# Performance work log

Hardware: AMD Instinct MI355X
Metric: run time of the kernel (lower is better)

The kernel has to match this reference:

```python
import jax, jax.numpy as jnp
import numpy as np

B, S, D, H = 2, 2048, 1024, 16
Dh = D // H
ROPE_BASE = 10000.0


def _rope_cos_sin(seq_len, dh, dtype):
    inv_freq = 1.0 / (ROPE_BASE ** (jnp.arange(0, dh, 2, dtype=jnp.float32) / dh))
    t = jnp.arange(seq_len, dtype=jnp.float32)
    freqs = jnp.outer(t, inv_freq)              # (S, Dh/2)
    emb = jnp.concatenate([freqs, freqs], -1)   # (S, Dh)
    return jnp.cos(emb).astype(dtype), jnp.sin(emb).astype(dtype)


def _rotate_half(x):
    x1, x2 = jnp.split(x, 2, axis=-1)
    return jnp.concatenate([-x2, x1], axis=-1)


def setup_inputs() -> dict:
    key = jax.random.key(0)
    k1, k2, k3 = jax.random.split(key, 3)
    x = jax.random.normal(k1, (B, S, D), dtype=jnp.float32)
    w_qkv = jax.random.normal(k2, (D, 3 * D), dtype=jnp.float32) * (1.0 / np.sqrt(D))
    w_proj = jax.random.normal(k3, (D, D), dtype=jnp.float32) * (1.0 / np.sqrt(D))
    return {"x": x, "w_qkv": w_qkv, "w_proj": w_proj}


def reference(x, w_qkv, w_proj):
    b, s, d = x.shape
    qkv = x @ w_qkv                              # (B, S, 3D)
    q, k, v = jnp.split(qkv, 3, axis=-1)
    # (B, S, D) -> (B, H, S, Dh)
    shape_heads = lambda t: t.reshape(b, s, H, Dh).transpose(0, 2, 1, 3)
    q, k, v = shape_heads(q), shape_heads(k), shape_heads(v)
    cos, sin = _rope_cos_sin(s, Dh, x.dtype)     # (S, Dh) each
    cos = cos[None, None]                        # (1,1,S,Dh)
    sin = sin[None, None]
    q = q * cos + _rotate_half(q) * sin
    k = k * cos + _rotate_half(k) * sin
    attn = jnp.einsum('bhqd,bhkd->bhqk', q, k) / np.sqrt(Dh).astype(x.dtype)
    causal_mask = jnp.tril(jnp.ones((s, s), dtype=bool))
    attn = jnp.where(causal_mask, attn, -jnp.inf)
    attn = jax.nn.softmax(attn, axis=-1)
    out = jnp.einsum('bhqk,bhkd->bhqd', attn, v)
    out = out.transpose(0, 2, 1, 3).reshape(b, s, d)
    return out @ w_proj
```

## Files before the change

kernel.cpp:

```cpp
#include <hip/hip_runtime.h>


typedef unsigned short u16;
typedef unsigned int u32;
typedef __bf16 bf16x8 __attribute__((ext_vector_type(8)));
typedef unsigned short u16x8 __attribute__((ext_vector_type(8)));
typedef unsigned short u16x4 __attribute__((ext_vector_type(4)));
typedef float f32x4 __attribute__((ext_vector_type(4)));

#define B_ 2
#define S_ 2048
#define D_ 1024
#define H_ 16
#define DH_ 64
#define BS_ (B_ * S_)
#define N3_ (3 * D_)

__device__ __forceinline__ u16 f2bf(float f) {
  unsigned u = __float_as_uint(f);
  u += 0x7FFFu + ((u >> 16) & 1u);
  return (u16)(u >> 16);
}
__device__ __forceinline__ float bf2f(u16 s) {
  return __uint_as_float(((unsigned)s) << 16);
}

union BU { u16x8 u; bf16x8 b; };

__device__ __forceinline__ void gl16(const void* g, void* l) {
  __builtin_amdgcn_global_load_lds(
      (const __attribute__((address_space(1))) u32*)g,
      (__attribute__((address_space(3))) u32*)l, 16, 0, 0);
}

__global__ __launch_bounds__(256) void k_pre(const float* __restrict__ x,
                                             const float* __restrict__ wqkv,
                                             const float* __restrict__ wproj,
                                             u16* __restrict__ xb,
                                             u16* __restrict__ wqkvT,
                                             u16* __restrict__ wprojT,
                                             float* __restrict__ ct,
                                             float* __restrict__ st) {
  __shared__ float tl[32][33];
  const int bid = blockIdx.x;
  const int t = threadIdx.x;
  if (bid < 4096) {
    const int i = bid * 256 + t;
    const float4 f = ((const float4*)x)[i];
    u16x4 o;
    o[0] = f2bf(f.x); o[1] = f2bf(f.y); o[2] = f2bf(f.z); o[3] = f2bf(f.w);
    *(u16x4*)(xb + (size_t)i * 4) = o;
    return;
  }
  if (bid < 8192) {
    const float* w; u16* wT; int R, C, bx, by;
    if (bid < 7168) {
      w = wqkv; wT = wqkvT; R = D_; C = N3_;
      const int id2 = bid - 4096; bx = id2 % 96; by = id2 / 96;
    } else {
      w = wproj; wT = wprojT; R = D_; C = D_;
      const int id2 = bid - 7168; bx = id2 % 32; by = id2 / 32;
    }
    const int lrow = t >> 3, seg = t & 7;
    const int r0 = by * 32, c0 = bx * 32;
    const float4 f = *(const float4*)(w + (size_t)(r0 + lrow) * C + c0 + seg * 4);
    tl[lrow][seg * 4 + 0] = f.x; tl[lrow][seg * 4 + 1] = f.y;
    tl[lrow][seg * 4 + 2] = f.z; tl[lrow][seg * 4 + 3] = f.w;
    __syncthreads();
    u16x4 o;
#pragma unroll
    for (int j = 0; j < 4; ++j) o[j] = f2bf(tl[seg * 4 + j][lrow]);
    *(u16x4*)(wT + (size_t)(c0 + lrow) * R + r0 + seg * 4) = o;
    return;
  }
  {
    const int idx = (bid - 8192) * 256 + t;
    const int tpos = idx >> 5, i = idx & 31;
    const float invf = powf(10000.0f, -(float)i * (1.0f / 32.0f));
    const float a = (float)tpos * invf;
    ct[idx] = cosf(a);
    st[idx] = sinf(a);
  }
}

template <typename OutT>
__global__ __launch_bounds__(256) void k_gemm(const u16* __restrict__ A,
                                              const u16* __restrict__ BT,
                                              OutT* __restrict__ C,
                                              int M, int N, int K, int nbx) {
  __shared__ u16 smem[16384];
  u16* laA = smem;
  u16* laB = smem + 8192;
  const int t = threadIdx.x;
  const int per_x = gridDim.x >> 3;
  const int nid = (blockIdx.x & 7) * per_x + (blockIdx.x >> 3);
  const int n0 = (nid % nbx) * 128, m0 = (nid / nbx) * 128;
  const int w = t >> 6, lane = t & 63;
  const int lr = lane & 15, lg = lane >> 4;
  const int wm = (w >> 1) * 64, wn = (w & 1) * 64;
  const int NK = K >> 5;

  const int srow = lane >> 2;
  const int sc = ((lane & 3) ^ ((lane >> 3) & 3)) * 8;
  const u16* Ag = A + (size_t)(m0 + w * 32 + srow) * K + sc;
  const u16* Bg = BT + (size_t)(n0 + w * 32 + srow) * K + sc;
  const int ldsw = w * 1024;

  f32x4 acc[4][4] = {};

#pragma unroll
  for (int i = 0; i < 2; ++i) {
    gl16(Ag + (size_t)i * 16 * K, laA + ldsw + i * 512);
    gl16(Bg + (size_t)i * 16 * K, laB + ldsw + i * 512);
  }
  __syncthreads();

  int cur = 0;
  for (int kt = 0; kt < NK; ++kt) {
    if (kt + 1 < NK) {
      const int ko = (kt + 1) * 32;
#pragma unroll
      for (int i = 0; i < 2; ++i) {
        gl16(Ag + (size_t)i * 16 * K + ko, laA + (cur ^ 1) * 4096 + ldsw + i * 512);
        gl16(Bg + (size_t)i * 16 * K + ko, laB + (cur ^ 1) * 4096 + ldsw + i * 512);
      }
    }
    const char* pa = (const char*)(laA + cur * 4096);
    const char* pb = (const char*)(laB + cur * 4096);
    BU af[4], bfr[4];
    const int rsw = ((lr >> 1) & 3);
#pragma unroll
    for (int mi = 0; mi < 4; ++mi) {
      const int ra = wm + mi * 16 + lr;
      af[mi].u = *(const u16x8*)(pa + ra * 64 + ((lg ^ rsw) * 16));
      const int rb = wn + mi * 16 + lr;
      bfr[mi].u = *(const u16x8*)(pb + rb * 64 + ((lg ^ rsw) * 16));
    }
#pragma unroll
    for (int mi = 0; mi < 4; ++mi)
#pragma unroll
      for (int ni = 0; ni < 4; ++ni)
        acc[mi][ni] = __builtin_amdgcn_mfma_f32_16x16x32_bf16(af[mi].b, bfr[ni].b,
                                                              acc[mi][ni], 0, 0, 0);
    __syncthreads();
    cur ^= 1;
  }

  if constexpr (sizeof(OutT) == 2) {
    u16* ew = smem + w * 4096;
#pragma unroll
    for (int mi = 0; mi < 4; ++mi)
#pragma unroll
      for (int ni = 0; ni < 4; ++ni)
#pragma unroll
        for (int r = 0; r < 4; ++r)
          ew[(mi * 16 + lg * 4 + r) * 64 + ni * 16 + lr] = f2bf(acc[mi][ni][r]);
    const int er = lane >> 3, es = (lane & 7) * 8;
#pragma unroll
    for (int pass = 0; pass < 8; ++pass) {
      const int row = pass * 8 + er;
      const u16x8 v = *(const u16x8*)(ew + row * 64 + es);
      *(u16x8*)((u16*)C + (size_t)(m0 + wm + row) * N + n0 + wn + es) = v;
    }
  } else {
#pragma unroll
    for (int mi = 0; mi < 4; ++mi)
#pragma unroll
      for (int ni = 0; ni < 4; ++ni)
#pragma unroll
        for (int r = 0; r < 4; ++r) {
          const int row = m0 + wm + mi * 16 + lg * 4 + r;
          const int col = n0 + wn + ni * 16 + lr;
          ((float*)C)[(size_t)row * N + col] = acc[mi][ni][r];
        }
  }
}

__global__ __launch_bounds__(256) void k_prep(const u16* __restrict__ qkv,
                                              const float* __restrict__ ct,
                                              const float* __restrict__ st,
                                              u16* __restrict__ Q, u16* __restrict__ K,
                                              u16* __restrict__ Vt) {
  __shared__ u16 vl[64][72];
  const int bid = blockIdx.x;
  const int xcd = bid & 7, slot = bid >> 3;
  const int bh = xcd + 8 * (slot >> 5);
  const int stile = slot & 31;
  const int b = bh >> 4, h = bh & 15;
  const int t = threadIdx.x;
  const int row = t >> 2, qr = t & 3;
  const int s = stile * 64 + row;
  const u16* base = qkv + (size_t)(b * S_ + s) * N3_ + h * DH_;
  const int d0 = qr * 8;
  float c[8], sn[8];
#pragma unroll
  for (int j = 0; j < 8; ++j) {
    c[j] = ct[s * 32 + d0 + j];
    sn[j] = st[s * 32 + d0 + j];
  }
#pragma unroll
  for (int part = 0; part < 2; ++part) {
    const float qs = (part == 0) ? 0.125f : 1.0f;
    const u16* src = base + part * D_;
    u16x8 lo = *(const u16x8*)(src + d0);
    u16x8 hi = *(const u16x8*)(src + d0 + 32);
    u16x8 olo, ohi;
#pragma unroll
    for (int j = 0; j < 8; ++j) {
      float x1 = bf2f(lo[j]) * qs, x2 = bf2f(hi[j]) * qs;
      olo[j] = f2bf(x1 * c[j] - x2 * sn[j]);
      ohi[j] = f2bf(x2 * c[j] + x1 * sn[j]);
    }
    u16* dst = (part ? K : Q) + ((size_t)bh * S_ + s) * DH_;
    *(u16x8*)(dst + d0) = olo;
    *(u16x8*)(dst + d0 + 32) = ohi;
  }
  u16x8 v0 = *(const u16x8*)(base + 2 * D_ + qr * 16);
  u16x8 v1 = *(const u16x8*)(base + 2 * D_ + qr * 16 + 8);
#pragma unroll
  for (int j = 0; j < 8; ++j) {
    vl[qr * 16 + j][row] = v0[j];
    vl[qr * 16 + 8 + j][row] = v1[j];
  }
  __syncthreads();
  const int dh = row, sc = qr * 16;
  u16x8 o0, o1;
#pragma unroll
  for (int j = 0; j < 8; ++j) { o0[j] = vl[dh][sc + j]; o1[j] = vl[dh][sc + 8 + j]; }
  u16* vdst = Vt + ((size_t)bh * DH_ + dh) * S_ + stile * 64 + sc;
  *(u16x8*)vdst = o0;
  *(u16x8*)(vdst + 8) = o1;
}

__global__ __launch_bounds__(256, 2) void k_attn(const u16* __restrict__ Q,
                                                 const u16* __restrict__ K,
                                                 const u16* __restrict__ Vt,
                                                 u16* __restrict__ Ao) {
  __shared__ char kvb_[2][16384];
  __shared__ char plb[4][2048];
  const int bid = blockIdx.x;
  const int xcd = bid & 7, inner = bid >> 3;
  const int bh = xcd + 8 * (inner & 3);
  const int qt = 31 - (inner >> 2);
  const int t = threadIdx.x;
  const int w = t >> 6, lane = t & 63;
  const int lr = lane & 15, lg = lane >> 4;
  const int q0 = qt * 64 + w * 16;
  const int nt = qt + 1;

  const u16* Kbh = K + (size_t)bh * S_ * DH_;
  const u16* Vbh = Vt + (size_t)bh * DH_ * S_;

  const int sr = lane >> 3;
  const int sc = ((lane & 7) ^ sr) * 8;
  char* kd0 = kvb_[0] + w * 2048;
  char* kd1 = kvb_[1] + w * 2048;

  const u16* Qb = Q + ((size_t)bh * S_ + q0) * DH_;
  BU qf0, qf1;
  qf0.u = *(const u16x8*)(Qb + lr * DH_ + lg * 8);
  qf1.u = *(const u16x8*)(Qb + lr * DH_ + 32 + lg * 8);

  f32x4 o[4] = {};
  float m = -1e30f, l = 0.f;
  char* plw = plb[w];
  const int psw = (lr & 7) << 4;

#pragma unroll
  for (int j = 0; j < 2; ++j) {
    const int row = w * 16 + j * 8 + sr;
    gl16(Kbh + (size_t)row * DH_ + sc, kd0 + j * 1024);
    gl16(Vbh + (size_t)row * S_ + sc, kd0 + 8192 + j * 1024);
  }
  __syncthreads();

  int cur = 0;
  for (int it = 0; it < nt; ++it) {
    const int kv0 = it * 64;
    if (it + 1 < nt) {
      const int kvn = kv0 + 64;
      char* nd = cur ? kd0 : kd1;
#pragma unroll
      for (int j = 0; j < 2; ++j) {
        const int row = w * 16 + j * 8 + sr;
        gl16(Kbh + (size_t)(kvn + row) * DH_ + sc, nd + j * 1024);
        gl16(Vbh + (size_t)row * S_ + kvn + sc, nd + 8192 + j * 1024);
      }
    }
    const char* base = kvb_[cur];
    f32x4 s[4] = {};
#pragma unroll
    for (int kvbi = 0; kvbi < 4; ++kvbi) {
      const int row = kvbi * 16 + lr;
      const int sw = (lr & 7) << 4;
      BU k0, k1;
      k0.u = *(const u16x8*)(base + row * 128 + ((lg * 16) ^ sw));
      k1.u = *(const u16x8*)(base + row * 128 + ((64 + lg * 16) ^ sw));
      s[kvbi] = __builtin_amdgcn_mfma_f32_16x16x32_bf16(k0.b, qf0.b, s[kvbi], 0, 0, 0);
      s[kvbi] = __builtin_amdgcn_mfma_f32_16x16x32_bf16(k1.b, qf1.b, s[kvbi], 0, 0, 0);
    }
    float p[16];
#pragma unroll
    for (int kvbi = 0; kvbi < 4; ++kvbi)
#pragma unroll
      for (int r = 0; r < 4; ++r) p[kvbi * 4 + r] = s[kvbi][r];
    if (it == nt - 1) {
#pragma unroll
      for (int kvbi = 0; kvbi < 4; ++kvbi)
#pragma unroll
        for (int r = 0; r < 4; ++r)
          if (kv0 + kvbi * 16 + lg * 4 + r > q0 + lr) p[kvbi * 4 + r] = -1e30f;
    }
    float mx = p[0];
#pragma unroll
    for (int i = 1; i < 16; ++i) mx = fmaxf(mx, p[i]);
    mx = fmaxf(mx, __shfl_xor(mx, 16, 64));
    mx = fmaxf(mx, __shfl_xor(mx, 32, 64));
    float al = 1.f;
    const bool resc = (mx > m + 8.f);
    if (resc) { al = __expf(m - mx); m = mx; }
    float sm = 0.f;
#pragma unroll
    for (int i = 0; i < 16; ++i) { p[i] = __expf(p[i] - m); sm += p[i]; }
    sm += __shfl_xor(sm, 16, 64);
    sm += __shfl_xor(sm, 32, 64);
    l = l * al + sm;
    if (resc) {
#pragma unroll
      for (int d = 0; d < 4; ++d)
#pragma unroll
        for (int r = 0; r < 4; ++r) o[d][r] *= al;
    }
#pragma unroll
    for (int kvbi = 0; kvbi < 4; ++kvbi) {
      u16x4 w4;
#pragma unroll
      for (int r = 0; r < 4; ++r) w4[r] = f2bf(p[kvbi * 4 + r]);
      *(u16x4*)(plw + lr * 128 + ((kvbi * 32 + lg * 8) ^ psw)) = w4;
    }
    BU pf0, pf1;
    pf0.u = *(const u16x8*)(plw + lr * 128 + ((lg * 16) ^ psw));
    pf1.u = *(const u16x8*)(plw + lr * 128 + ((64 + lg * 16) ^ psw));
#pragma unroll
    for (int d = 0; d < 4; ++d) {
      const int row = d * 16 + lr;
      const int sw = (lr & 7) << 4;
      BU v0, v1;
      v0.u = *(const u16x8*)(base + 8192 + row * 128 + ((lg * 16) ^ sw));
      v1.u = *(const u16x8*)(base + 8192 + row * 128 + ((64 + lg * 16) ^ sw));
      o[d] = __builtin_amdgcn_mfma_f32_16x16x32_bf16(v0.b, pf0.b, o[d], 0, 0, 0);
      o[d] = __builtin_amdgcn_mfma_f32_16x16x32_bf16(v1.b, pf1.b, o[d], 0, 0, 0);
    }
    __syncthreads();
    cur ^= 1;
  }

  const float inv = 1.0f / l;
  const int b = bh >> 4, h = bh & 15;
  const size_t rowo = ((size_t)b * S_ + q0 + lr) * D_ + h * DH_;
#pragma unroll
  for (int d = 0; d < 4; ++d) {
    u16x4 w4;
#pragma unroll
    for (int r = 0; r < 4; ++r) w4[r] = f2bf(o[d][r] * inv);
    *(u16x4*)(Ao + rowo + d * 16 + lg * 4) = w4;
  }
}

extern "C" void kernel_launch(void* const* d_in, const int* in_sizes, int n_in,
                              void* d_out, int out_size, void* d_ws, size_t ws_size,
                              hipStream_t stream) {
  const float* x = (const float*)d_in[0];
  const float* wqkv = (const float*)d_in[1];
  const float* wproj = (const float*)d_in[2];
  float* out = (float*)d_out;
  char* ws = (char*)d_ws;

  u16* xb      = (u16*)(ws + 0);
  u16* wqkvT   = (u16*)(ws + 8388608);
  u16* wprojT  = (u16*)(ws + 14680064);
  u16* qkvb    = (u16*)(ws + 16777216);
  u16* Qb      = (u16*)(ws + 41943040);
  u16* Kb      = (u16*)(ws + 50331648);
  u16* Vtb     = (u16*)(ws + 58720256);
  u16* aob     = (u16*)(ws + 67108864);
  float* ct    = (float*)(ws + 75497472);
  float* stab  = (float*)(ws + 75759616);

  k_pre<<<8448, 256, 0, stream>>>(x, wqkv, wproj, xb, wqkvT, wprojT, ct, stab);
  k_gemm<u16><<<768, 256, 0, stream>>>(xb, wqkvT, qkvb, BS_, N3_, D_, 24);
  k_prep<<<1024, 256, 0, stream>>>(qkvb, ct, stab, Qb, Kb, Vtb);
  k_attn<<<1024, 256, 0, stream>>>(Qb, Kb, Vtb, aob);
  k_gemm<float><<<256, 256, 0, stream>>>(aob, wprojT, out, BS_, D_, D_, 8);
}
```

Baseline: 119.4 us.

## Permute K rows so P stays in registers, skip LDS round-trip for PV

K tiles are now loaded with a permuted row order, so each lane's QK^T accumulator outputs already sit in the layout needed for the P operand of the PV MFMA. P is then packed into bf16 registers directly instead of being written to and read back from a per-wave LDS buffer. The causal mask index is remapped to match the permutation. The row sum is kept per lane and reduced across lanes only once at the end. The rescale branch is now taken wave-uniformly via __any, which saves shuffles per tile and removes the P staging buffer at the cost of trickier index bookkeeping.

```diff
diff --git a/kernel.cpp b/kernel.cpp
--- a/kernel.cpp
+++ b/kernel.cpp
@@ -25,7 +25,7 @@
   return __uint_as_float(((unsigned)s) << 16);
 }
 
-union BU { u16x8 u; bf16x8 b; };
+union BU { u16x8 u; bf16x8 b; u32 w[4]; };
 
 __device__ __forceinline__ void gl16(const void* g, void* l) {
   __builtin_amdgcn_global_load_lds(
@@ -237,7 +237,6 @@
                                                  const u16* __restrict__ Vt,
                                                  u16* __restrict__ Ao) {
   __shared__ char kvb_[2][16384];
-  __shared__ char plb[4][2048];
   const int bid = blockIdx.x;
   const int xcd = bid & 7, inner = bid >> 3;
   const int bh = xcd + 8 * (inner & 3);
@@ -255,6 +254,14 @@
   const int sc = ((lane & 7) ^ sr) * 8;
   char* kd0 = kvb_[0] + w * 2048;
   char* kd1 = kvb_[1] + w * 2048;
+  int prow[2], vrow[2];
+#pragma unroll
+  for (int j = 0; j < 2; ++j) {
+    const int a = w * 16 + j * 8 + sr;
+    prow[j] = (((a >> 4) & 1) << 5) | (((a >> 2) & 3) << 3) |
+              (((a >> 5) & 1) << 2) | (a & 3);
+    vrow[j] = a;
+  }
 
   const u16* Qb = Q + ((size_t)bh * S_ + q0) * DH_;
   BU qf0, qf1;
@@ -263,14 +270,11 @@
 
   f32x4 o[4] = {};
   float m = -1e30f, l = 0.f;
-  char* plw = plb[w];
-  const int psw = (lr & 7) << 4;
 
 #pragma unroll
   for (int j = 0; j < 2; ++j) {
-    const int row = w * 16 + j * 8 + sr;
-    gl16(Kbh + (size_t)row * DH_ + sc, kd0 + j * 1024);
-    gl16(Vbh + (size_t)row * S_ + sc, kd0 + 8192 + j * 1024);
+    gl16(Kbh + (size_t)prow[j] * DH_ + sc, kd0 + j * 1024);
+    gl16(Vbh + (size_t)vrow[j] * S_ + sc, kd0 + 8192 + j * 1024);
   }
   __syncthreads();
 
@@ -282,9 +286,8 @@
       char* nd = cur ? kd0 : kd1;
 #pragma unroll
       for (int j = 0; j < 2; ++j) {
-        const int row = w * 16 + j * 8 + sr;
-        gl16(Kbh + (size_t)(kvn + row) * DH_ + sc, nd + j * 1024);
-        gl16(Vbh + (size_t)row * S_ + kvn + sc, nd + 8192 + j * 1024);
+        gl16(Kbh + (size_t)(kvn + prow[j]) * DH_ + sc, nd + j * 1024);
+        gl16(Vbh + (size_t)vrow[j] * S_ + kvn + sc, nd + 8192 + j * 1024);
       }
     }
     const char* base = kvb_[cur];
@@ -308,39 +311,48 @@
 #pragma unroll
       for (int kvbi = 0; kvbi < 4; ++kvbi)
 #pragma unroll
-        for (int r = 0; r < 4; ++r)
-          if (kv0 + kvbi * 16 + lg * 4 + r > q0 + lr) p[kvbi * 4 + r] = -1e30f;
-    }
-    float mx = p[0];
-#pragma unroll
-    for (int i = 1; i < 16; ++i) mx = fmaxf(mx, p[i]);
-    mx = fmaxf(mx, __shfl_xor(mx, 16, 64));
-    mx = fmaxf(mx, __shfl_xor(mx, 32, 64));
-    float al = 1.f;
-    const bool resc = (mx > m + 8.f);
-    if (resc) { al = __expf(m - mx); m = mx; }
-    float sm = 0.f;
-#pragma unroll
-    for (int i = 0; i < 16; ++i) { p[i] = __expf(p[i] - m); sm += p[i]; }
-    sm += __shfl_xor(sm, 16, 64);
-    sm += __shfl_xor(sm, 32, 64);
-    l = l * al + sm;
-    if (resc) {
+        for (int r = 0; r < 4; ++r) {
+          const int tkv = ((kvbi & 1) << 5) + lg * 8 + ((kvbi >> 1) << 2) + r;
+          if (kv0 + tkv > q0 + lr) p[kvbi * 4 + r] = -1e30f;
+        }
+    }
+    float a0 = fmaxf(p[0], p[1]),   a1 = fmaxf(p[2], p[3]);
+    float a2 = fmaxf(p[4], p[5]),   a3 = fmaxf(p[6], p[7]);
+    float a4 = fmaxf(p[8], p[9]),   a5 = fmaxf(p[10], p[11]);
+    float a6 = fmaxf(p[12], p[13]), a7 = fmaxf(p[14], p[15]);
+    a0 = fmaxf(a0, a1); a2 = fmaxf(a2, a3); a4 = fmaxf(a4, a5); a6 = fmaxf(a6, a7);
+    const float mx = fmaxf(fmaxf(a0, a2), fmaxf(a4, a6));
+    if (__any(mx > m + 8.f)) {
+      float cm = mx;
+      cm = fmaxf(cm, __shfl_xor(cm, 16, 64));
+      cm = fmaxf(cm, __shfl_xor(cm, 32, 64));
+      const float mn = fmaxf(m, cm);
+      const float al = __expf(m - mn);
+      m = mn;
+      l *= al;
 #pragma unroll
       for (int d = 0; d < 4; ++d)
 #pragma unroll
         for (int r = 0; r < 4; ++r) o[d][r] *= al;
     }
 #pragma unroll
-    for (int kvbi = 0; kvbi < 4; ++kvbi) {
-      u16x4 w4;
-#pragma unroll
-      for (int r = 0; r < 4; ++r) w4[r] = f2bf(p[kvbi * 4 + r]);
-      *(u16x4*)(plw + lr * 128 + ((kvbi * 32 + lg * 8) ^ psw)) = w4;
+    for (int i = 0; i < 16; ++i) p[i] = __expf(p[i] - m);
+    {
+      float s0 = (p[0] + p[1]) + (p[2] + p[3]);
+      float s1 = (p[4] + p[5]) + (p[6] + p[7]);
+      float s2 = (p[8] + p[9]) + (p[10] + p[11]);
+      float s3 = (p[12] + p[13]) + (p[14] + p[15]);
+      l += (s0 + s1) + (s2 + s3);
     }
     BU pf0, pf1;
-    pf0.u = *(const u16x8*)(plw + lr * 128 + ((lg * 16) ^ psw));
-    pf1.u = *(const u16x8*)(plw + lr * 128 + ((64 + lg * 16) ^ psw));
+    pf0.u[0] = f2bf(p[0]);  pf0.u[1] = f2bf(p[1]);
+    pf0.u[2] = f2bf(p[2]);  pf0.u[3] = f2bf(p[3]);
+    pf0.u[4] = f2bf(p[8]);  pf0.u[5] = f2bf(p[9]);
+    pf0.u[6] = f2bf(p[10]); pf0.u[7] = f2bf(p[11]);
+    pf1.u[0] = f2bf(p[4]);  pf1.u[1] = f2bf(p[5]);
+    pf1.u[2] = f2bf(p[6]);  pf1.u[3] = f2bf(p[7]);
+    pf1.u[4] = f2bf(p[12]); pf1.u[5] = f2bf(p[13]);
+    pf1.u[6] = f2bf(p[14]); pf1.u[7] = f2bf(p[15]);
 #pragma unroll
     for (int d = 0; d < 4; ++d) {
       const int row = d * 16 + lr;
@@ -355,6 +367,8 @@
     cur ^= 1;
   }
 
+  l += __shfl_xor(l, 16, 64);
+  l += __shfl_xor(l, 32, 64);
   const float inv = 1.0f / l;
   const int b = bh >> 4, h = bh & 15;
   const size_t rowo = ((size_t)b * S_ + q0 + lr) * D_ + h * DH_;
```

After: 110.7 us. 7.3% less time.
